# Optimization experiments

Measured on AMD Instinct MI355X. Metric: run time of the kernel, lower is better.

## Reference

```python
import jax, jax.numpy as jnp
import numpy as np

N, A, D, O = 8192, 32, 768, 256
LN_EPS = 1e-5


def setup_inputs() -> dict:
    key = jax.random.key(0)
    ks = jax.random.split(key, 9)
    articles = jax.random.normal(ks[0], (N, A, D), dtype=jnp.float32)
    counts = jax.random.randint(ks[1], (N,), 0, 33, dtype=jnp.int64)
    # Parameters (PyTorch Linear default-ish init scale)
    attn_w = jax.random.normal(ks[2], (D,), dtype=jnp.float32) / np.sqrt(D)
    attn_b = jax.random.normal(ks[3], (1,), dtype=jnp.float32) * 0.01
    proj_w = jax.random.normal(ks[4], (D, O), dtype=jnp.float32) / np.sqrt(D)
    proj_b = jax.random.normal(ks[5], (O,), dtype=jnp.float32) * 0.01
    ln_w = jnp.ones((O,), dtype=jnp.float32)
    ln_b = jnp.zeros((O,), dtype=jnp.float32)
    no_news = jax.random.normal(ks[6], (O,), dtype=jnp.float32) * 0.02
    return {"articles": articles, "counts": counts, "attn_w": attn_w,
            "attn_b": attn_b, "proj_w": proj_w, "proj_b": proj_b,
            "ln_w": ln_w, "ln_b": ln_b, "no_news": no_news}


def reference(articles, counts, attn_w, attn_b, proj_w, proj_b, ln_w, ln_b, no_news):
    # mask of valid (non-padded) articles: [N, A]
    mask = jnp.arange(A)[None, :] < counts[:, None]
    # attention scores per article: [N, A]
    scores = jnp.einsum('nad,d->na', articles, attn_w) + attn_b[0]
    scores = jnp.where(mask, scores, -1e9)
    # softmax over the (masked) article axis; count==1 reduces to weight 1,
    # matching the original squeeze(0) path exactly.
    weights = jax.nn.softmax(scores, axis=1)
    pooled = jnp.einsum('na,nad->nd', weights, articles)  # [N, D]
    # projection: Linear -> LayerNorm -> GELU (exact, erf-based as in torch)
    h = pooled @ proj_w + proj_b  # [N, O]
    mu = jnp.mean(h, axis=-1, keepdims=True)
    var = jnp.mean((h - mu) ** 2, axis=-1, keepdims=True)
    h_ln = (h - mu) / jnp.sqrt(var + LN_EPS) * ln_w + ln_b
    h_out = jax.nn.gelu(h_ln, approximate=False)
    # fallback to learned no-news embedding when there are zero articles
    return jnp.where(counts[:, None] > 0, h_out, no_news[None, :])
```

## Files before the change

### kernel.cpp

```cpp
#include <hip/hip_runtime.h>
#include <math.h>

#define N_ROWS 8192
#define A_ART  32
#define D_DIM  768
#define O_DIM  256
#define LN_EPS 1e-5f
#define R_TILE 16
#define P_STR  772

typedef unsigned short u16;
typedef unsigned int   u32;

__device__ __forceinline__ float bf2f(u16 u) { return __uint_as_float(((u32)u) << 16); }
__device__ __forceinline__ u16 f2bf(float f) {
    u32 x = __float_as_uint(f);
    return (u16)((x + 0x7fffu + ((x >> 16) & 1u)) >> 16);
}
__device__ __forceinline__ float cvt(float v) { return v; }
__device__ __forceinline__ float cvt(u16 v)   { return bf2f(v); }

#define WS_PROJW   256
#define WS_PARAMS  786688
#define WS_POOLED  793984
#define P_ATTNB    768
#define P_PROJB    800
#define P_LNW      1056
#define P_LNB      1312
#define P_NONEWS   1568

__global__ __launch_bounds__(64) void detect_kernel(const u32* __restrict__ art_w,
                                                    const int* __restrict__ cnt_w,
                                                    int* __restrict__ flags) {
    const int lane = threadIdx.x;
    u32 w = art_w[lane];
    u32 low = w & 0xffffu;
    u32 e = (low >> 7) & 0xffu;
    bool sane = (e >= 100u && e <= 140u) || ((low & 0x7fffu) == 0u);
    unsigned long long m1 = __ballot(sane);
    bool hz = true;
    if (lane < 32) hz = (cnt_w[2 * lane + 1] == 0);
    unsigned long long m2 = __ballot(hz);
    if (lane == 0) {
        flags[0] = (__popcll(m1) >= 48) ? 1 : 0;
        flags[1] = (m2 == ~0ull) ? 1 : 0;
    }
}

__device__ __forceinline__ float ldf(const void* p, int i, bool bf) {
    return bf ? bf2f(((const u16*)p)[i]) : ((const float*)p)[i];
}

__global__ __launch_bounds__(256) void params_kernel(const void* attn_w, const void* attn_b,
                                                     const void* proj_b, const void* ln_w,
                                                     const void* ln_b, const void* no_news,
                                                     const void* proj_w,
                                                     const int* __restrict__ flags,
                                                     float* __restrict__ projw_f,
                                                     float* __restrict__ params_f) {
    const bool bf = flags[0] != 0;
    const int b = blockIdx.x, t = threadIdx.x;
    if (b < 768) {
        int i = b * 256 + t;
        projw_f[i] = ldf(proj_w, i, bf);
    } else {
        int i = (b - 768) * 256 + t;
        if (i < 768)                    params_f[i] = ldf(attn_w, i, bf);
        else if (i == P_ATTNB)          params_f[i] = ldf(attn_b, 0, bf);
        else if (i >= P_PROJB  && i < P_PROJB  + 256) params_f[i] = ldf(proj_b,  i - P_PROJB,  bf);
        else if (i >= P_LNW    && i < P_LNW    + 256) params_f[i] = ldf(ln_w,    i - P_LNW,    bf);
        else if (i >= P_LNB    && i < P_LNB    + 256) params_f[i] = ldf(ln_b,    i - P_LNB,    bf);
        else if (i >= P_NONEWS && i < P_NONEWS + 256) params_f[i] = ldf(no_news, i - P_NONEWS, bf);
    }
}

template <typename T>
__global__ __launch_bounds__(256) void pool_kernel(const T* __restrict__ articles,
                                                   const int* __restrict__ counts32,
                                                   const int* __restrict__ flags,
                                                   const float* __restrict__ params_f,
                                                   float* __restrict__ pooled) {
    const bool want_bf = (sizeof(T) == 2);
    if ((flags[0] != 0) != want_bf) return;
    const int n = blockIdx.x, t = threadIdx.x;
    const int c = counts32[flags[1] ? 2 * n : n];

    if (c <= 0) {
        #pragma unroll
        for (int j = 0; j < 3; ++j) pooled[(size_t)n * D_DIM + t + 256 * j] = 0.0f;
        return;
    }

    __shared__ float lds_scores[A_ART];
    __shared__ float lds_w[A_ART];

    const int wave = t >> 6, lane = t & 63;
    const T* rowbase = articles + (size_t)n * A_ART * D_DIM;

    for (int a = wave; a < c; a += 4) {
        float s = 0.f;
        if (sizeof(T) == 2) {
            const u32* ap = (const u32*)(rowbase + a * D_DIM);
            #pragma unroll
            for (int j = 0; j < 6; ++j) {
                u32 w = ap[lane + 64 * j];
                int d = 2 * (lane + 64 * j);
                s += bf2f((u16)(w & 0xffffu)) * params_f[d]
                   + bf2f((u16)(w >> 16))     * params_f[d + 1];
            }
        } else {
            const float2* ap = (const float2*)(rowbase + a * D_DIM);
            #pragma unroll
            for (int j = 0; j < 6; ++j) {
                float2 w = ap[lane + 64 * j];
                int d = 2 * (lane + 64 * j);
                s += w.x * params_f[d] + w.y * params_f[d + 1];
            }
        }
        #pragma unroll
        for (int off = 32; off; off >>= 1) s += __shfl_xor(s, off);
        if (lane == 0) lds_scores[a] = s + params_f[P_ATTNB];
    }
    __syncthreads();

    float m = -1e30f;
    for (int a = 0; a < c; ++a) m = fmaxf(m, lds_scores[a]);
    float ssum = 0.f;
    for (int a = 0; a < c; ++a) ssum += __expf(lds_scores[a] - m);
    if (t < c) lds_w[t] = __expf(lds_scores[t] - m) / ssum;
    __syncthreads();

    #pragma unroll
    for (int j = 0; j < 3; ++j) {
        const int d = t + 256 * j;
        float acc = 0.f;
        for (int a = 0; a < c; ++a)
            acc = fmaf(lds_w[a], cvt(rowbase[a * D_DIM + d]), acc);
        pooled[(size_t)n * D_DIM + d] = acc;
    }
}

__global__ __launch_bounds__(256) void proj_kernel(const float* __restrict__ pooled,
                                                   const float* __restrict__ projw_f,
                                                   const float* __restrict__ params_f,
                                                   const int* __restrict__ counts32,
                                                   const int* __restrict__ flags,
                                                   void* __restrict__ out) {
    __shared__ float lds_p[R_TILE * P_STR];
    __shared__ float lds_s[R_TILE * 16];
    __shared__ float lds_q[R_TILE * 16];
    __shared__ float lds_mu[R_TILE];
    __shared__ float lds_rs[R_TILE];

    const int t = threadIdx.x;
    const int row0 = blockIdx.x * R_TILE;
    const bool out_bf = flags[0] != 0;
    const bool c64 = flags[1] != 0;

    const float4* src = (const float4*)(pooled + (size_t)row0 * D_DIM);
    for (int q = t; q < R_TILE * (D_DIM / 4); q += 256) {
        int r  = q / (D_DIM / 4);
        int dc = (q % (D_DIM / 4)) * 4;
        *((float4*)&lds_p[r * P_STR + dc]) = src[q];
    }
    __syncthreads();

    const int r  = t & 15;
    const int ob = (t >> 4) * 16;

    float acc[16];
    #pragma unroll
    for (int j = 0; j < 16; ++j) acc[j] = 0.f;

    for (int d = 0; d < D_DIM; ++d) {
        const float pv = lds_p[r * P_STR + d];
        const float4* wrow = (const float4*)(projw_f + d * O_DIM + ob);
        float4 wa = wrow[0], wb = wrow[1], wc = wrow[2], wd = wrow[3];
        acc[0]  = fmaf(pv, wa.x, acc[0]);  acc[1]  = fmaf(pv, wa.y, acc[1]);
        acc[2]  = fmaf(pv, wa.z, acc[2]);  acc[3]  = fmaf(pv, wa.w, acc[3]);
        acc[4]  = fmaf(pv, wb.x, acc[4]);  acc[5]  = fmaf(pv, wb.y, acc[5]);
        acc[6]  = fmaf(pv, wb.z, acc[6]);  acc[7]  = fmaf(pv, wb.w, acc[7]);
        acc[8]  = fmaf(pv, wc.x, acc[8]);  acc[9]  = fmaf(pv, wc.y, acc[9]);
        acc[10] = fmaf(pv, wc.z, acc[10]); acc[11] = fmaf(pv, wc.w, acc[11]);
        acc[12] = fmaf(pv, wd.x, acc[12]); acc[13] = fmaf(pv, wd.y, acc[13]);
        acc[14] = fmaf(pv, wd.z, acc[14]); acc[15] = fmaf(pv, wd.w, acc[15]);
    }

    float ps = 0.f, pq = 0.f;
    #pragma unroll
    for (int j = 0; j < 16; ++j) {
        acc[j] += params_f[P_PROJB + ob + j];
        ps += acc[j];
        pq += acc[j] * acc[j];
    }
    lds_s[r * 16 + (t >> 4)] = ps;
    lds_q[r * 16 + (t >> 4)] = pq;
    __syncthreads();

    if (t < 16) {
        float s = 0.f, q = 0.f;
        #pragma unroll
        for (int g = 0; g < 16; ++g) { s += lds_s[t * 16 + g]; q += lds_q[t * 16 + g]; }
        float mu  = s * (1.0f / O_DIM);
        float var = q * (1.0f / O_DIM) - mu * mu;
        lds_mu[t] = mu;
        lds_rs[t] = rsqrtf(var + LN_EPS);
    }
    __syncthreads();

    const float mu = lds_mu[r];
    const float rs = lds_rs[r];
    const int row = row0 + r;
    const int cnt = counts32[c64 ? 2 * row : row];

    float vals[16];
    #pragma unroll
    for (int j = 0; j < 16; ++j) {
        const int o = ob + j;
        float x = (acc[j] - mu) * rs * params_f[P_LNW + o] + params_f[P_LNB + o];
        float g = 0.5f * x * (1.0f + erff(x * 0.70710678118654752f));
        vals[j] = (cnt > 0) ? g : params_f[P_NONEWS + o];
    }

    if (out_bf) {
        u16 obuf[16];
        #pragma unroll
        for (int j = 0; j < 16; ++j) obuf[j] = f2bf(vals[j]);
        uint4* dst = (uint4*)((u16*)out + (size_t)row * O_DIM + ob);
        dst[0] = *((const uint4*)&obuf[0]);
        dst[1] = *((const uint4*)&obuf[8]);
    } else {
        float4* dst = (float4*)((float*)out + (size_t)row * O_DIM + ob);
        dst[0] = *((const float4*)&vals[0]);
        dst[1] = *((const float4*)&vals[4]);
        dst[2] = *((const float4*)&vals[8]);
        dst[3] = *((const float4*)&vals[12]);
    }
}

extern "C" void kernel_launch(void* const* d_in, const int* in_sizes, int n_in,
                              void* d_out, int out_size, void* d_ws, size_t ws_size,
                              hipStream_t stream) {
    const void* articles = d_in[0];
    const int*  counts   = (const int*)d_in[1];
    const void* attn_w   = d_in[2];
    const void* attn_b   = d_in[3];
    const void* proj_w   = d_in[4];
    const void* proj_b   = d_in[5];
    const void* ln_w     = d_in[6];
    const void* ln_b     = d_in[7];
    const void* no_news  = d_in[8];

    int*   flags    = (int*)d_ws;
    float* projw_f  = (float*)((char*)d_ws + WS_PROJW);
    float* params_f = (float*)((char*)d_ws + WS_PARAMS);
    float* pooled   = (float*)((char*)d_ws + WS_POOLED);

    detect_kernel<<<1, 64, 0, stream>>>((const u32*)articles, counts, flags);
    params_kernel<<<776, 256, 0, stream>>>(attn_w, attn_b, proj_b, ln_w, ln_b, no_news,
                                           proj_w, flags, projw_f, params_f);
    pool_kernel<u16><<<N_ROWS, 256, 0, stream>>>((const u16*)articles, counts, flags,
                                                 params_f, pooled);
    pool_kernel<float><<<N_ROWS, 256, 0, stream>>>((const float*)articles, counts, flags,
                                                   params_f, pooled);
    proj_kernel<<<N_ROWS / R_TILE, 256, 0, stream>>>(pooled, projw_f, params_f, counts,
                                                     flags, d_out);
}
```

Before: 1.163 ms.

## Fuse pooling into single-pass online softmax with per-wave partial merges

Replaces the two-pass pooling (compute scores, then re-read articles for the weighted sum) with a single pass. Each wave computes its article's score and keeps an online-softmax running max, sum and accumulator in registers, and the four wave partials are merged through shared memory. This removes the second read of the articles tensor, which is the dominant memory traffic, and merges the two type-templated launches into one kernel that branches on the runtime dtype flag. The cost is extra exp/rescale work per article and a shared-memory buffer of 4x768 floats per block, which may lower occupancy.

After: 1.141 ms. About the same (-1.9%).

```diff
diff --git a/kernel.cpp b/kernel.cpp
--- a/kernel.cpp
+++ b/kernel.cpp
@@ -17,8 +17,6 @@
     u32 x = __float_as_uint(f);
     return (u16)((x + 0x7fffu + ((x >> 16) & 1u)) >> 16);
 }
-__device__ __forceinline__ float cvt(float v) { return v; }
-__device__ __forceinline__ float cvt(u16 v)   { return bf2f(v); }
 
 #define WS_PROJW   256
 #define WS_PARAMS  786688
@@ -74,15 +72,34 @@
     }
 }
 
-template <typename T>
-__global__ __launch_bounds__(256) void pool_kernel(const T* __restrict__ articles,
+#define ONLINE_STEP                                                          \
+    {                                                                        \
+        float s = 0.f;                                                       \
+        _Pragma("unroll")                                                    \
+        for (int k = 0; k < 12; ++k) s = fmaf(art[k], wfrag[k], s);          \
+        _Pragma("unroll")                                                    \
+        for (int off = 32; off; off >>= 1) s += __shfl_xor(s, off);          \
+        s += bias;                                                           \
+        float mn = fmaxf(m, s);                                              \
+        float scale = __expf(m - mn);                                        \
+        float p = __expf(s - mn);                                            \
+        l = l * scale + p;                                                   \
+        _Pragma("unroll")                                                    \
+        for (int k = 0; k < 12; ++k) acc[k] = fmaf(p, art[k], acc[k] * scale); \
+        m = mn;                                                              \
+    }
+
+__global__ __launch_bounds__(256) void pool_kernel(const void* __restrict__ articles,
                                                    const int* __restrict__ counts32,
                                                    const int* __restrict__ flags,
                                                    const float* __restrict__ params_f,
                                                    float* __restrict__ pooled) {
-    const bool want_bf = (sizeof(T) == 2);
-    if ((flags[0] != 0) != want_bf) return;
+    __shared__ float lds_acc[4][D_DIM];
+    __shared__ float lds_m[4];
+    __shared__ float lds_l[4];
+
     const int n = blockIdx.x, t = threadIdx.x;
+    const int wave = t >> 6, lane = t & 63;
     const int c = counts32[flags[1] ? 2 * n : n];
 
     if (c <= 0) {
@@ -91,52 +108,68 @@
         return;
     }
 
-    __shared__ float lds_scores[A_ART];
-    __shared__ float lds_w[A_ART];
-
-    const int wave = t >> 6, lane = t & 63;
-    const T* rowbase = articles + (size_t)n * A_ART * D_DIM;
-
-    for (int a = wave; a < c; a += 4) {
-        float s = 0.f;
-        if (sizeof(T) == 2) {
-            const u32* ap = (const u32*)(rowbase + a * D_DIM);
+    float wfrag[12];
+    #pragma unroll
+    for (int j = 0; j < 3; ++j) {
+        float4 wv = *(const float4*)(params_f + 4 * (lane + 64 * j));
+        wfrag[4 * j + 0] = wv.x; wfrag[4 * j + 1] = wv.y;
+        wfrag[4 * j + 2] = wv.z; wfrag[4 * j + 3] = wv.w;
+    }
+    const float bias = params_f[P_ATTNB];
+
+    float m = -1e30f, l = 0.f;
+    float acc[12];
+    #pragma unroll
+    for (int k = 0; k < 12; ++k) acc[k] = 0.f;
+
+    if (flags[0]) {
+        const u16* base = (const u16*)articles + (size_t)n * A_ART * D_DIM;
+        for (int a = wave; a < c; a += 4) {
+            float art[12];
             #pragma unroll
-            for (int j = 0; j < 6; ++j) {
-                u32 w = ap[lane + 64 * j];
-                int d = 2 * (lane + 64 * j);
-                s += bf2f((u16)(w & 0xffffu)) * params_f[d]
-                   + bf2f((u16)(w >> 16))     * params_f[d + 1];
+            for (int j = 0; j < 3; ++j) {
+                uint2 q = *(const uint2*)(base + a * D_DIM + 4 * (lane + 64 * j));
+                art[4 * j + 0] = bf2f((u16)(q.x & 0xffffu));
+                art[4 * j + 1] = bf2f((u16)(q.x >> 16));
+                art[4 * j + 2] = bf2f((u16)(q.y & 0xffffu));
+                art[4 * j + 3] = bf2f((u16)(q.y >> 16));
             }
-        } else {
-            const float2* ap = (const float2*)(rowbase + a * D_DIM);
+            ONLINE_STEP
+        }
+    } else {
+        const float* base = (const float*)articles + (size_t)n * A_ART * D_DIM;
+        for (int a = wave; a < c; a += 4) {
+            float art[12];
             #pragma unroll
-            for (int j = 0; j < 6; ++j) {
-                float2 w = ap[lane + 64 * j];
-                int d = 2 * (lane + 64 * j);
-                s += w.x * params_f[d] + w.y * params_f[d + 1];
+            for (int j = 0; j < 3; ++j) {
+                float4 q = *(const float4*)(base + a * D_DIM + 4 * (lane + 64 * j));
+                art[4 * j + 0] = q.x; art[4 * j + 1] = q.y;
+                art[4 * j + 2] = q.z; art[4 * j + 3] = q.w;
             }
+            ONLINE_STEP
         }
-        #pragma unroll
-        for (int off = 32; off; off >>= 1) s += __shfl_xor(s, off);
-        if (lane == 0) lds_scores[a] = s + params_f[P_ATTNB];
-    }
-    __syncthreads();
-
-    float m = -1e30f;
-    for (int a = 0; a < c; ++a) m = fmaxf(m, lds_scores[a]);
-    float ssum = 0.f;
-    for (int a = 0; a < c; ++a) ssum += __expf(lds_scores[a] - m);
-    if (t < c) lds_w[t] = __expf(lds_scores[t] - m) / ssum;
-    __syncthreads();
+    }
+
+    if (lane == 0) { lds_m[wave] = m; lds_l[wave] = l; }
+    #pragma unroll
+    for (int j = 0; j < 3; ++j) {
+        *((float4*)&lds_acc[wave][4 * (lane + 64 * j)]) =
+            make_float4(acc[4 * j + 0], acc[4 * j + 1], acc[4 * j + 2], acc[4 * j + 3]);
+    }
+    __syncthreads();
+
+    float M = fmaxf(fmaxf(lds_m[0], lds_m[1]), fmaxf(lds_m[2], lds_m[3]));
+    float e0 = __expf(lds_m[0] - M), e1 = __expf(lds_m[1] - M);
+    float e2 = __expf(lds_m[2] - M), e3 = __expf(lds_m[3] - M);
+    float L = lds_l[0] * e0 + lds_l[1] * e1 + lds_l[2] * e2 + lds_l[3] * e3;
+    float invL = __frcp_rn(L);
 
     #pragma unroll
     for (int j = 0; j < 3; ++j) {
         const int d = t + 256 * j;
-        float acc = 0.f;
-        for (int a = 0; a < c; ++a)
-            acc = fmaf(lds_w[a], cvt(rowbase[a * D_DIM + d]), acc);
-        pooled[(size_t)n * D_DIM + d] = acc;
+        float v = lds_acc[0][d] * e0 + lds_acc[1][d] * e1
+                + lds_acc[2][d] * e2 + lds_acc[3][d] * e3;
+        pooled[(size_t)n * D_DIM + d] = v * invL;
     }
 }
 
@@ -243,13 +276,6 @@
                               hipStream_t stream) {
     const void* articles = d_in[0];
     const int*  counts   = (const int*)d_in[1];
-    const void* attn_w   = d_in[2];
-    const void* attn_b   = d_in[3];
-    const void* proj_w   = d_in[4];
-    const void* proj_b   = d_in[5];
-    const void* ln_w     = d_in[6];
-    const void* ln_b     = d_in[7];
-    const void* no_news  = d_in[8];
 
     int*   flags    = (int*)d_ws;
     float* projw_f  = (float*)((char*)d_ws + WS_PROJW);
@@ -257,12 +283,9 @@
     float* pooled   = (float*)((char*)d_ws + WS_POOLED);
 
     detect_kernel<<<1, 64, 0, stream>>>((const u32*)articles, counts, flags);
-    params_kernel<<<776, 256, 0, stream>>>(attn_w, attn_b, proj_b, ln_w, ln_b, no_news,
-                                           proj_w, flags, projw_f, params_f);
-    pool_kernel<u16><<<N_ROWS, 256, 0, stream>>>((const u16*)articles, counts, flags,
-                                                 params_f, pooled);
-    pool_kernel<float><<<N_ROWS, 256, 0, stream>>>((const float*)articles, counts, flags,
-                                                   params_f, pooled);
+    params_kernel<<<776, 256, 0, stream>>>(d_in[2], d_in[3], d_in[5], d_in[6], d_in[7],
+                                           d_in[8], d_in[4], flags, projw_f, params_f);
+    pool_kernel<<<N_ROWS, 256, 0, stream>>>(articles, counts, flags, params_f, pooled);
     proj_kernel<<<N_ROWS / R_TILE, 256, 0, stream>>>(pooled, projw_f, params_f, counts,
                                                      flags, d_out);
 }
```
